# Kernel optimization log

Hardware: AMD Instinct MI355X
Metric: run time of the kernel (lower is better)

The kernel has to match this reference:

```python
import jax, jax.numpy as jnp
import numpy as np

B, S, D = 1, 2048, 4096
H, KVH, HD = 32, 8, 128
GROUPS = H // KVH  # 4
SCALE = HD ** -0.5
NEG = jnp.finfo(jnp.float32).min


def rotate_half(x):
    x1 = x[..., : x.shape[-1] // 2]
    x2 = x[..., x.shape[-1] // 2:]
    return jnp.concatenate((-x2, x1), axis=-1)


def setup_inputs() -> dict:
    key = jax.random.key(0)
    ks = jax.random.split(key, 8)
    return {
        "hidden_states": jax.random.normal(ks[0], (B, S, D), dtype=jnp.float32),
        "cos": jax.random.uniform(ks[1], (B, S, HD), dtype=jnp.float32),
        "sin": jax.random.uniform(ks[2], (B, S, HD), dtype=jnp.float32),
        "attention_mask": jnp.ones((B, S), dtype=bool),
        "wq": jax.random.normal(ks[3], (D, H * HD), dtype=jnp.float32) * 0.02,
        "wk": jax.random.normal(ks[4], (D, KVH * HD), dtype=jnp.float32) * 0.02,
        "wv": jax.random.normal(ks[5], (D, KVH * HD), dtype=jnp.float32) * 0.02,
        "wo": jax.random.normal(ks[6], (H * HD, D), dtype=jnp.float32) * 0.02,
    }


def reference(hidden_states, cos, sin, attention_mask, wq, wk, wv, wo):
    b, s, _ = hidden_states.shape
    # projections -> (B,S,heads,head_dim)
    q = (hidden_states @ wq).reshape(b, s, H, HD)
    k = (hidden_states @ wk).reshape(b, s, KVH, HD)
    v = (hidden_states @ wv).reshape(b, s, KVH, HD)
    # RoPE (cos/sin unsqueezed at head axis)
    c = cos[:, :, None, :]
    si = sin[:, :, None, :]
    q = q * c + rotate_half(q) * si
    k = k * c + rotate_half(k) * si
    # GQA: repeat kv heads (cache_index=0, max_len==S -> cache write is identity)
    k = jnp.repeat(k, GROUPS, axis=2)
    v = jnp.repeat(v, GROUPS, axis=2)
    # mask: causal AND padding; bias 0 / -inf
    causal = jnp.tril(jnp.ones((s, s), dtype=bool))[None, None]  # (1,1,S,S)
    mask = causal & attention_mask[:, None, None, :]  # (B,1,S,S)
    bias = jnp.where(mask, 0.0, NEG).astype(hidden_states.dtype)
    # scores (B,H,S,S)
    scores = jnp.einsum("bqhd,bkhd->bhqk", q, k) * SCALE + bias
    attn = jax.nn.softmax(scores, axis=-1)
    out = jnp.einsum("bhqk,bkhd->bqhd", attn, v).reshape(b, s, H * HD)
    return out @ wo
```

## Files before the change

### kernel.cpp

```cpp
#include <hip/hip_runtime.h>
#include <hip/hip_bf16.h>

#define SEQ   2048
#define DM    4096
#define NH    32
#define NKVH  8
#define HD    128
#define NQKV  6144
#define KOFF  4096
#define VOFF  5120
#define SCALE 0.08838834764831845f

typedef __attribute__((ext_vector_type(4))) float f32x4;
typedef __attribute__((ext_vector_type(8))) short short8;

__device__ __forceinline__ unsigned short f2bf(float f) {
  union { float f; unsigned int u; } v; v.f = f;
  unsigned int r = v.u + 0x7FFF + ((v.u >> 16) & 1);
  return (unsigned short)(r >> 16);
}
__device__ __forceinline__ float bf2f(unsigned short b) {
  union { unsigned int u; float f; } v; v.u = ((unsigned int)b) << 16;
  return v.f;
}

__device__ __forceinline__ void gld16(const unsigned short* g, unsigned short* l) {
  __builtin_amdgcn_global_load_lds(
      (const __attribute__((address_space(1))) unsigned int*)g,
      (__attribute__((address_space(3))) unsigned int*)l, 16, 0, 0);
}

__global__ __launch_bounds__(256) void cast_f32_bf16(const float* __restrict__ in,
                                                     unsigned short* __restrict__ out) {
  size_t i = ((size_t)blockIdx.x * 256 + threadIdx.x) * 4;
  float4 v = *(const float4*)(in + i);
  ushort4 o;
  o.x = f2bf(v.x); o.y = f2bf(v.y); o.z = f2bf(v.z); o.w = f2bf(v.w);
  *(ushort4*)(out + i) = o;
}

__global__ __launch_bounds__(256) void transpose_cast(const float* __restrict__ W,
                                                      unsigned short* __restrict__ Wt,
                                                      int K, int N, int row_off) {
  __shared__ float tile[32][33];
  int n0 = blockIdx.x * 32, k0 = blockIdx.y * 32;
  int x = threadIdx.x & 31, y4 = (threadIdx.x >> 5) * 4;
#pragma unroll
  for (int i = 0; i < 4; ++i)
    tile[y4 + i][x] = W[(size_t)(k0 + y4 + i) * N + n0 + x];
  __syncthreads();
#pragma unroll
  for (int i = 0; i < 4; ++i)
    Wt[(size_t)(row_off + n0 + y4 + i) * K + k0 + x] = f2bf(tile[x][y4 + i]);
}

__global__ __launch_bounds__(256) void v_transpose(const unsigned short* __restrict__ QKV,
                                                   unsigned short* __restrict__ Vt_g) {
  __shared__ unsigned short t[32][33];
  int s0 = blockIdx.x * 32, c0 = blockIdx.y * 32;
  int x = threadIdx.x & 31, y4 = (threadIdx.x >> 5) * 4;
#pragma unroll
  for (int i = 0; i < 4; ++i)
    t[y4 + i][x] = QKV[(size_t)(s0 + y4 + i) * NQKV + VOFF + c0 + x];
  __syncthreads();
#pragma unroll
  for (int i = 0; i < 4; ++i)
    Vt_g[(size_t)(c0 + y4 + i) * SEQ + s0 + x] = t[x][y4 + i];
}

__global__ __launch_bounds__(256) void gemm_bt(const unsigned short* __restrict__ A,
                                               const unsigned short* __restrict__ Bt,
                                               void* __restrict__ C,
                                               int M, int N, int K, int c_fp32) {
  __shared__ unsigned short As[128 * 32];
  __shared__ unsigned short Bs[128 * 32];
  const int tid  = threadIdx.x;
  const int m0   = blockIdx.y * 128;
  const int n0   = blockIdx.x * 128;
  const int w    = tid >> 6;
  const int lane = tid & 63;
  const int l16  = lane & 15;
  const int quad = lane >> 4;
  const int wr   = (w >> 1) * 64;
  const int wc   = (w & 1) * 64;

  f32x4 acc[4][4];
#pragma unroll
  for (int i = 0; i < 4; ++i)
#pragma unroll
    for (int j = 0; j < 4; ++j) acc[i][j] = (f32x4){0.f, 0.f, 0.f, 0.f};

  const int sr  = lane >> 2;
  const int pb  = lane & 3;
  const int sws = (sr & 3) ^ ((sr >> 2) & 3);
  const int kb  = ((pb ^ sws) << 3);
  const unsigned short* ga0 = A  + (size_t)(m0 + w * 16 + sr) * K + kb;
  const unsigned short* ga1 = A  + (size_t)(m0 + 64 + w * 16 + sr) * K + kb;
  const unsigned short* gb0 = Bt + (size_t)(n0 + w * 16 + sr) * K + kb;
  const unsigned short* gb1 = Bt + (size_t)(n0 + 64 + w * 16 + sr) * K + kb;
  unsigned short* la0 = As + (w * 16) * 32;
  unsigned short* la1 = As + (64 + w * 16) * 32;
  unsigned short* lb0 = Bs + (w * 16) * 32;
  unsigned short* lb1 = Bs + (64 + w * 16) * 32;

  const int swf  = (l16 & 3) ^ ((l16 >> 2) & 3);
  const int fcol = ((quad ^ swf) << 3);

  for (int k0 = 0; k0 < K; k0 += 32) {
    __syncthreads();
    gld16(ga0 + k0, la0);
    gld16(ga1 + k0, la1);
    gld16(gb0 + k0, lb0);
    gld16(gb1 + k0, lb1);
    __syncthreads();
    short8 af[4], bfr[4];
#pragma unroll
    for (int mt = 0; mt < 4; ++mt)
      af[mt] = *(const short8*)&As[(wr + mt * 16 + l16) * 32 + fcol];
#pragma unroll
    for (int nt = 0; nt < 4; ++nt)
      bfr[nt] = *(const short8*)&Bs[(wc + nt * 16 + l16) * 32 + fcol];
#pragma unroll
    for (int mt = 0; mt < 4; ++mt)
#pragma unroll
      for (int nt = 0; nt < 4; ++nt)
        acc[mt][nt] = __builtin_amdgcn_mfma_f32_16x16x32_bf16(af[mt], bfr[nt], acc[mt][nt], 0, 0, 0);
  }

  if (c_fp32) {
    float* Cf = (float*)C;
#pragma unroll
    for (int mt = 0; mt < 4; ++mt)
#pragma unroll
      for (int nt = 0; nt < 4; ++nt) {
        int col = n0 + wc + nt * 16 + l16;
#pragma unroll
        for (int r = 0; r < 4; ++r)
          Cf[(size_t)(m0 + wr + mt * 16 + quad * 4 + r) * N + col] = acc[mt][nt][r];
      }
  } else {
    unsigned short* Cb = (unsigned short*)C;
#pragma unroll
    for (int mt = 0; mt < 4; ++mt)
#pragma unroll
      for (int nt = 0; nt < 4; ++nt) {
        int col = n0 + wc + nt * 16 + l16;
#pragma unroll
        for (int r = 0; r < 4; ++r)
          Cb[(size_t)(m0 + wr + mt * 16 + quad * 4 + r) * N + col] = f2bf(acc[mt][nt][r]);
      }
  }
}

__global__ __launch_bounds__(256) void rope_kernel(unsigned short* __restrict__ QKV,
                                                   const float* __restrict__ cosb,
                                                   const float* __restrict__ sinb) {
  int idx = blockIdx.x * 256 + threadIdx.x;
  int i = idx & 63;
  int h = (idx >> 6) % 40;
  int s = idx / 2560;
  size_t base = (size_t)s * NQKV + (size_t)h * 128;
  float q1 = bf2f(QKV[base + i]);
  float q2 = bf2f(QKV[base + i + 64]);
  float c1 = cosb[s * 128 + i],      s1 = sinb[s * 128 + i];
  float c2 = cosb[s * 128 + i + 64], s2 = sinb[s * 128 + i + 64];
  QKV[base + i]      = f2bf(q1 * c1 - q2 * s1);
  QKV[base + i + 64] = f2bf(q2 * c2 + q1 * s2);
}

__global__ __launch_bounds__(256) void flash_attn(const unsigned short* __restrict__ QKV,
                                                  const unsigned short* __restrict__ Vt_g,
                                                  unsigned short* __restrict__ AO) {
  __shared__ unsigned short Ks[64 * 136];
  __shared__ unsigned short Vs[128 * 72];
  __shared__ unsigned short Ps[4][32 * 68];

  const int h   = blockIdx.x;
  const int qt  = (int)gridDim.y - 1 - (int)blockIdx.y;
  const int kvh = h >> 2;
  const int tid  = threadIdx.x;
  const int w    = tid >> 6;
  const int lane = tid & 63;
  const int l16  = lane & 15;
  const int quad = lane >> 4;
  const int q0   = qt * 128;
  const int qrow_w = q0 + w * 32;

  short8 qf[2][4];
#pragma unroll
  for (int ntq = 0; ntq < 2; ++ntq) {
    const unsigned short* qp = QKV + (size_t)(qrow_w + ntq * 16 + l16) * NQKV + h * HD + quad * 8;
#pragma unroll
    for (int ks = 0; ks < 4; ++ks) qf[ntq][ks] = *(const short8*)(qp + ks * 32);
  }

  f32x4 o[8][2];
#pragma unroll
  for (int i = 0; i < 8; ++i) { o[i][0] = (f32x4){0,0,0,0}; o[i][1] = (f32x4){0,0,0,0}; }
  float m_i[2] = {-3.0e38f, -3.0e38f}, l_i[2] = {0.f, 0.f};

  const int kr = tid >> 2, kcol0 = (tid & 3) * 32;
  const int vr = tid >> 1, vcol0 = (tid & 1) * 32;
  const unsigned short* kbase = QKV + KOFF + (size_t)kvh * HD + kcol0;
  const unsigned short* vbase = Vt_g + ((size_t)kvh * HD + vr) * SEQ + vcol0;

  const int nch = qt * 2 + 2;
  for (int c = 0; c < nch; ++c) {
    const int kc = c * 64;
    short8 kv[4], vv[4];
#pragma unroll
    for (int u = 0; u < 4; ++u) kv[u] = *(const short8*)(kbase + (size_t)(kc + kr) * NQKV + u * 8);
#pragma unroll
    for (int u = 0; u < 4; ++u) vv[u] = *(const short8*)(vbase + kc + u * 8);
    __syncthreads();
#pragma unroll
    for (int u = 0; u < 4; ++u) *(short8*)&Ks[kr * 136 + kcol0 + u * 8] = kv[u];
#pragma unroll
    for (int u = 0; u < 4; ++u) *(short8*)&Vs[vr * 72 + vcol0 + u * 8] = vv[u];
    __syncthreads();

    if (kc <= qrow_w + 31) {
      f32x4 st[4][2];
#pragma unroll
      for (int mt = 0; mt < 4; ++mt) { st[mt][0] = (f32x4){0,0,0,0}; st[mt][1] = (f32x4){0,0,0,0}; }
#pragma unroll
      for (int ks = 0; ks < 4; ++ks)
#pragma unroll
        for (int mt = 0; mt < 4; ++mt) {
          short8 ak = *(const short8*)&Ks[(mt * 16 + l16) * 136 + ks * 32 + quad * 8];
          st[mt][0] = __builtin_amdgcn_mfma_f32_16x16x32_bf16(ak, qf[0][ks], st[mt][0], 0, 0, 0);
          st[mt][1] = __builtin_amdgcn_mfma_f32_16x16x32_bf16(ak, qf[1][ks], st[mt][1], 0, 0, 0);
        }

      float sc[4][2][4];
#pragma unroll
      for (int mt = 0; mt < 4; ++mt)
#pragma unroll
        for (int ntq = 0; ntq < 2; ++ntq) {
          int qr = qrow_w + ntq * 16 + l16;
#pragma unroll
          for (int r = 0; r < 4; ++r) {
            int key = kc + mt * 16 + quad * 4 + r;
            float v = st[mt][ntq][r] * SCALE;
            sc[mt][ntq][r] = (key <= qr) ? v : -__builtin_inff();
          }
        }
      float mx[2] = {-__builtin_inff(), -__builtin_inff()};
#pragma unroll
      for (int mt = 0; mt < 4; ++mt)
#pragma unroll
        for (int ntq = 0; ntq < 2; ++ntq)
#pragma unroll
          for (int r = 0; r < 4; ++r) mx[ntq] = fmaxf(mx[ntq], sc[mt][ntq][r]);
#pragma unroll
      for (int ntq = 0; ntq < 2; ++ntq) {
        mx[ntq] = fmaxf(mx[ntq], __shfl_xor(mx[ntq], 16, 64));
        mx[ntq] = fmaxf(mx[ntq], __shfl_xor(mx[ntq], 32, 64));
      }
      float al[2], mn[2];
#pragma unroll
      for (int ntq = 0; ntq < 2; ++ntq) {
        mn[ntq] = fmaxf(m_i[ntq], mx[ntq]);
        al[ntq] = __expf(m_i[ntq] - mn[ntq]);
        m_i[ntq] = mn[ntq];
      }

      float rs[2] = {0.f, 0.f};
      unsigned short* psw = &Ps[w][0];
#pragma unroll
      for (int mt = 0; mt < 4; ++mt)
#pragma unroll
        for (int ntq = 0; ntq < 2; ++ntq) {
          float p0 = __expf(sc[mt][ntq][0] - mn[ntq]);
          float p1 = __expf(sc[mt][ntq][1] - mn[ntq]);
          float p2 = __expf(sc[mt][ntq][2] - mn[ntq]);
          float p3 = __expf(sc[mt][ntq][3] - mn[ntq]);
          rs[ntq] += (p0 + p1) + (p2 + p3);
          ushort4 pk; pk.x = f2bf(p0); pk.y = f2bf(p1); pk.z = f2bf(p2); pk.w = f2bf(p3);
          *(ushort4*)&psw[(ntq * 16 + l16) * 68 + mt * 16 + quad * 4] = pk;
        }
#pragma unroll
      for (int ntq = 0; ntq < 2; ++ntq) {
        rs[ntq] += __shfl_xor(rs[ntq], 16, 64);
        rs[ntq] += __shfl_xor(rs[ntq], 32, 64);
        l_i[ntq] = l_i[ntq] * al[ntq] + rs[ntq];
      }
#pragma unroll
      for (int i = 0; i < 8; ++i) {
        o[i][0][0] *= al[0]; o[i][0][1] *= al[0]; o[i][0][2] *= al[0]; o[i][0][3] *= al[0];
        o[i][1][0] *= al[1]; o[i][1][1] *= al[1]; o[i][1][2] *= al[1]; o[i][1][3] *= al[1];
      }

#pragma unroll
      for (int ks = 0; ks < 2; ++ks) {
        short8 bp[2];
#pragma unroll
        for (int ntq = 0; ntq < 2; ++ntq) {
          union { ushort4 h[2]; short8 v; } u;
          const unsigned short* pp = &psw[(ntq * 16 + l16) * 68 + ks * 32 + quad * 8];
          u.h[0] = *(const ushort4*)(pp);
          u.h[1] = *(const ushort4*)(pp + 4);
          bp[ntq] = u.v;
        }
#pragma unroll
        for (int mt = 0; mt < 8; ++mt) {
          short8 av = *(const short8*)&Vs[(mt * 16 + l16) * 72 + ks * 32 + quad * 8];
          o[mt][0] = __builtin_amdgcn_mfma_f32_16x16x32_bf16(av, bp[0], o[mt][0], 0, 0, 0);
          o[mt][1] = __builtin_amdgcn_mfma_f32_16x16x32_bf16(av, bp[1], o[mt][1], 0, 0, 0);
        }
      }
    }
  }

  float inv[2] = {1.0f / l_i[0], 1.0f / l_i[1]};
#pragma unroll
  for (int mt = 0; mt < 8; ++mt)
#pragma unroll
    for (int ntq = 0; ntq < 2; ++ntq) {
      int qr = qrow_w + ntq * 16 + l16;
      int col = h * HD + mt * 16 + quad * 4;
      ushort4 ov;
      ov.x = f2bf(o[mt][ntq][0] * inv[ntq]);
      ov.y = f2bf(o[mt][ntq][1] * inv[ntq]);
      ov.z = f2bf(o[mt][ntq][2] * inv[ntq]);
      ov.w = f2bf(o[mt][ntq][3] * inv[ntq]);
      *(ushort4*)&AO[(size_t)qr * DM + col] = ov;
    }
}

extern "C" void kernel_launch(void* const* d_in, const int* in_sizes, int n_in,
                              void* d_out, int out_size, void* d_ws, size_t ws_size,
                              hipStream_t stream) {
  const float* hs   = (const float*)d_in[0];
  const float* cosb = (const float*)d_in[1];
  const float* sinb = (const float*)d_in[2];
  const float* wq = (const float*)d_in[4];
  const float* wk = (const float*)d_in[5];
  const float* wv = (const float*)d_in[6];
  const float* wo = (const float*)d_in[7];
  float* out = (float*)d_out;

  char* ws = (char*)d_ws;
  unsigned short* hsb   = (unsigned short*)(ws);
  unsigned short* wqkvT = (unsigned short*)(ws + (16u << 20));
  unsigned short* woT   = (unsigned short*)(ws + (64u << 20));
  unsigned short* qkv   = (unsigned short*)(ws + (96u << 20));
  unsigned short* ao    = (unsigned short*)(ws + (120u << 20));
  unsigned short* Vt_g  = hsb;

  cast_f32_bf16<<<8192, 256, 0, stream>>>(hs, hsb);
  transpose_cast<<<dim3(128, 128), 256, 0, stream>>>(wq, wqkvT, 4096, 4096, 0);
  transpose_cast<<<dim3(32, 128), 256, 0, stream>>>(wk, wqkvT, 4096, 1024, 4096);
  transpose_cast<<<dim3(32, 128), 256, 0, stream>>>(wv, wqkvT, 4096, 1024, 5120);
  transpose_cast<<<dim3(128, 128), 256, 0, stream>>>(wo, woT, 4096, 4096, 0);

  gemm_bt<<<dim3(NQKV / 128, SEQ / 128), 256, 0, stream>>>(hsb, wqkvT, qkv, SEQ, NQKV, DM, 0);
  rope_kernel<<<20480, 256, 0, stream>>>(qkv, cosb, sinb);
  v_transpose<<<dim3(64, 32), 256, 0, stream>>>(qkv, Vt_g);
  flash_attn<<<dim3(NH, SEQ / 128), 256, 0, stream>>>(qkv, Vt_g, ao);
  gemm_bt<<<dim3(DM / 128, SEQ / 128), 256, 0, stream>>>(ao, woT, out, SEQ, DM, DM, 1);
}
```

Before: 573.2 us.

## Merge weight transpose-casts into one kernel and use fragment-major GEMM LDS layout

Replaces the four per-weight transpose_cast launches with a single transpose_all kernel. It uses 64x64 tiles, float4 loads and ushort4 stores, with the bf16 conversion done before the shared-memory stage. The GEMM's shared tiles are reorganised into per-16-row fragment blocks: each lane loads its 16-byte chunk directly into LDS in MFMA fragment order and reads it back at lane*8, replacing the XOR swizzle. The aim is fewer launches, wider memory accesses in the weight preprocessing, and simpler conflict-free LDS reads in the GEMM. The risk is that the new LDS write pattern may change bank behaviour or the coalescing of global loads.

```diff
diff --git a/kernel.cpp b/kernel.cpp
--- a/kernel.cpp
+++ b/kernel.cpp
@@ -39,19 +39,40 @@
   *(ushort4*)(out + i) = o;
 }
 
-__global__ __launch_bounds__(256) void transpose_cast(const float* __restrict__ W,
-                                                      unsigned short* __restrict__ Wt,
-                                                      int K, int N, int row_off) {
-  __shared__ float tile[32][33];
-  int n0 = blockIdx.x * 32, k0 = blockIdx.y * 32;
-  int x = threadIdx.x & 31, y4 = (threadIdx.x >> 5) * 4;
-#pragma unroll
-  for (int i = 0; i < 4; ++i)
-    tile[y4 + i][x] = W[(size_t)(k0 + y4 + i) * N + n0 + x];
+__global__ __launch_bounds__(256) void transpose_all(const float* __restrict__ wq,
+                                                     const float* __restrict__ wk,
+                                                     const float* __restrict__ wv,
+                                                     const float* __restrict__ wo,
+                                                     unsigned short* __restrict__ wqkvT,
+                                                     unsigned short* __restrict__ woT) {
+  __shared__ unsigned short t[64][68];
+  const int bx = blockIdx.x;
+  const float* W; unsigned short* out; int N, n0, row_off;
+  if (bx < 64)      { W = wq; out = wqkvT; N = 4096; n0 = bx * 64;        row_off = 0;    }
+  else if (bx < 80) { W = wk; out = wqkvT; N = 1024; n0 = (bx - 64) * 64; row_off = 4096; }
+  else if (bx < 96) { W = wv; out = wqkvT; N = 1024; n0 = (bx - 80) * 64; row_off = 5120; }
+  else              { W = wo; out = woT;   N = 4096; n0 = (bx - 96) * 64; row_off = 0;    }
+  const int k0 = blockIdx.y * 64;
+  const int tid = threadIdx.x;
+
+  const int lr = tid >> 4, lc = (tid & 15) * 4;
+#pragma unroll
+  for (int i = 0; i < 4; ++i) {
+    float4 v = *(const float4*)&W[(size_t)(k0 + lr + i * 16) * N + n0 + lc];
+    ushort4 u; u.x = f2bf(v.x); u.y = f2bf(v.y); u.z = f2bf(v.z); u.w = f2bf(v.w);
+    *(ushort4*)&t[lr + i * 16][lc] = u;
+  }
   __syncthreads();
-#pragma unroll
-  for (int i = 0; i < 4; ++i)
-    Wt[(size_t)(row_off + n0 + y4 + i) * K + k0 + x] = f2bf(tile[x][y4 + i]);
+
+  const int sn = tid >> 2, sk = (tid & 3) * 4;
+#pragma unroll
+  for (int i = 0; i < 4; ++i) {
+    int kk = sk + i * 16;
+    ushort4 u;
+    u.x = t[kk + 0][sn]; u.y = t[kk + 1][sn];
+    u.z = t[kk + 2][sn]; u.w = t[kk + 3][sn];
+    *(ushort4*)&out[(size_t)(row_off + n0 + sn) * DM + k0 + kk] = u;
+  }
 }
 
 __global__ __launch_bounds__(256) void v_transpose(const unsigned short* __restrict__ QKV,
@@ -72,8 +93,8 @@
                                                const unsigned short* __restrict__ Bt,
                                                void* __restrict__ C,
                                                int M, int N, int K, int c_fp32) {
-  __shared__ unsigned short As[128 * 32];
-  __shared__ unsigned short Bs[128 * 32];
+  __shared__ unsigned short As[8][512];
+  __shared__ unsigned short Bs[8][512];
   const int tid  = threadIdx.x;
   const int m0   = blockIdx.y * 128;
   const int n0   = blockIdx.x * 128;
@@ -90,36 +111,28 @@
 #pragma unroll
     for (int j = 0; j < 4; ++j) acc[i][j] = (f32x4){0.f, 0.f, 0.f, 0.f};
 
-  const int sr  = lane >> 2;
-  const int pb  = lane & 3;
-  const int sws = (sr & 3) ^ ((sr >> 2) & 3);
-  const int kb  = ((pb ^ sws) << 3);
-  const unsigned short* ga0 = A  + (size_t)(m0 + w * 16 + sr) * K + kb;
-  const unsigned short* ga1 = A  + (size_t)(m0 + 64 + w * 16 + sr) * K + kb;
-  const unsigned short* gb0 = Bt + (size_t)(n0 + w * 16 + sr) * K + kb;
-  const unsigned short* gb1 = Bt + (size_t)(n0 + 64 + w * 16 + sr) * K + kb;
-  unsigned short* la0 = As + (w * 16) * 32;
-  unsigned short* la1 = As + (64 + w * 16) * 32;
-  unsigned short* lb0 = Bs + (w * 16) * 32;
-  unsigned short* lb1 = Bs + (64 + w * 16) * 32;
-
-  const int swf  = (l16 & 3) ^ ((l16 >> 2) & 3);
-  const int fcol = ((quad ^ swf) << 3);
+  const int f0 = 2 * w, f1 = 2 * w + 1;
+  const unsigned short* gA0 = A  + (size_t)(m0 + f0 * 16 + l16) * K + quad * 8;
+  const unsigned short* gA1 = A  + (size_t)(m0 + f1 * 16 + l16) * K + quad * 8;
+  const unsigned short* gB0 = Bt + (size_t)(n0 + f0 * 16 + l16) * K + quad * 8;
+  const unsigned short* gB1 = Bt + (size_t)(n0 + f1 * 16 + l16) * K + quad * 8;
+  unsigned short* lA0 = &As[f0][0];
+  unsigned short* lA1 = &As[f1][0];
+  unsigned short* lB0 = &Bs[f0][0];
+  unsigned short* lB1 = &Bs[f1][0];
+  const int fa = wr >> 4, fb = wc >> 4;
 
   for (int k0 = 0; k0 < K; k0 += 32) {
     __syncthreads();
-    gld16(ga0 + k0, la0);
-    gld16(ga1 + k0, la1);
-    gld16(gb0 + k0, lb0);
-    gld16(gb1 + k0, lb1);
+    gld16(gA0, lA0); gld16(gA1, lA1);
+    gld16(gB0, lB0); gld16(gB1, lB1);
+    gA0 += 32; gA1 += 32; gB0 += 32; gB1 += 32;
     __syncthreads();
     short8 af[4], bfr[4];
 #pragma unroll
-    for (int mt = 0; mt < 4; ++mt)
-      af[mt] = *(const short8*)&As[(wr + mt * 16 + l16) * 32 + fcol];
-#pragma unroll
-    for (int nt = 0; nt < 4; ++nt)
-      bfr[nt] = *(const short8*)&Bs[(wc + nt * 16 + l16) * 32 + fcol];
+    for (int mt = 0; mt < 4; ++mt) af[mt]  = *(const short8*)&As[fa + mt][lane * 8];
+#pragma unroll
+    for (int nt = 0; nt < 4; ++nt) bfr[nt] = *(const short8*)&Bs[fb + nt][lane * 8];
 #pragma unroll
     for (int mt = 0; mt < 4; ++mt)
 #pragma unroll
@@ -349,10 +362,7 @@
   unsigned short* Vt_g  = hsb;
 
   cast_f32_bf16<<<8192, 256, 0, stream>>>(hs, hsb);
-  transpose_cast<<<dim3(128, 128), 256, 0, stream>>>(wq, wqkvT, 4096, 4096, 0);
-  transpose_cast<<<dim3(32, 128), 256, 0, stream>>>(wk, wqkvT, 4096, 1024, 4096);
-  transpose_cast<<<dim3(32, 128), 256, 0, stream>>>(wv, wqkvT, 4096, 1024, 5120);
-  transpose_cast<<<dim3(128, 128), 256, 0, stream>>>(wo, woT, 4096, 4096, 0);
+  transpose_all<<<dim3(160, 64), 256, 0, stream>>>(wq, wk, wv, wo, wqkvT, woT);
 
   gemm_bt<<<dim3(NQKV / 128, SEQ / 128), 256, 0, stream>>>(hsb, wqkvT, qkv, SEQ, NQKV, DM, 0);
   rope_kernel<<<20480, 256, 0, stream>>>(qkv, cosb, sinb);
```

Result: slower. 645.2 us (+12.6%).
